# Kernel optimization log

Measured on AMD Instinct MI355X. Metric: run time of the kernel, lower is better.

The kernel has to match this reference:

```python
import jax, jax.numpy as jnp
import numpy as np

L, B, S, D, H, DH, V = 6, 2048, 64, 256, 8, 64, 100
INNER = H * DH          # 512
FF = 4 * D              # 1024 (GeGLU hidden after chunk)
SCALE = 8.0             # sqrt(DH)


def setup_inputs() -> dict:
    key = jax.random.key(0)
    ks = jax.random.split(key, 8)
    s = 0.02
    return {
        "x": jax.random.randint(ks[0], (B, S), 0, V),
        "E": jax.random.normal(ks[1], (S, V, D), dtype=jnp.float32) * s,
        "ln1_g": jnp.ones((L, D), jnp.float32),
        "ln1_b": jnp.zeros((L, D), jnp.float32),
        "Wqkv": jax.random.normal(ks[2], (L, D, 3 * INNER), dtype=jnp.float32) * s,
        "Wout": jax.random.normal(ks[3], (L, INNER, D), dtype=jnp.float32) * s,
        "bout": jnp.zeros((L, D), jnp.float32),
        "ln2_g": jnp.ones((L, D), jnp.float32),
        "ln2_b": jnp.zeros((L, D), jnp.float32),
        "W1": jax.random.normal(ks[4], (L, D, 2 * FF), dtype=jnp.float32) * s,
        "b1": jnp.zeros((L, 2 * FF), jnp.float32),
        "W2": jax.random.normal(ks[5], (L, FF, D), dtype=jnp.float32) * s,
        "b2": jnp.zeros((L, D), jnp.float32),
    }


def _ln(x, g, b):
    m = x.mean(-1, keepdims=True)
    v = ((x - m) ** 2).mean(-1, keepdims=True)
    return (x - m) * jax.lax.rsqrt(v + 1e-5) * g + b


def _split_heads(t):
    # [B,S,H*DH] -> [B,H,S,DH]
    return t.reshape(B, S, H, DH).transpose(0, 2, 1, 3)


def reference(x, E, ln1_g, ln1_b, Wqkv, Wout, bout, ln2_g, ln2_b, W1, b1, W2, b2):
    # per-column embedding lookup: E[col, x[b,col]] -> [B,S,D]
    h = E[jnp.arange(S)[None, :], x]
    for l in range(L):
        # PreNorm -> MHA
        n = _ln(h, ln1_g[l], ln1_b[l])
        qkv = n @ Wqkv[l]
        q, k, v = jnp.split(qkv, 3, axis=-1)
        q, k, v = _split_heads(q), _split_heads(k), _split_heads(v)
        score = jax.nn.softmax(
            jnp.einsum("bhqd,bhkd->bhqk", q, k) / SCALE, axis=-1
        )
        o = jnp.einsum("bhqk,bhkd->bhqd", score, v)
        o = o.transpose(0, 2, 1, 3).reshape(B, S, INNER)
        h = h + o @ Wout[l] + bout[l]
        # PreNorm -> GeGLU FFN
        n2 = _ln(h, ln2_g[l], ln2_b[l])
        u = n2 @ W1[l] + b1[l]
        a, g = jnp.split(u, 2, axis=-1)
        h = (a * jax.nn.gelu(g, approximate=False)) @ W2[l] + b2[l] + h
    return h
```

## Files before the change

### kernel.cpp

```cpp
#include <hip/hip_runtime.h>
#include <stdint.h>
#include <math.h>


#define LAYERS 6
#define BATCH  2048
#define SEQ    64
#define DMODEL 256
#define NHEAD  8
#define INNERD 512
#define FFDIM  1024
#define VOCAB  100
#define MTOK   (BATCH*SEQ)
#define MCAP   65536

typedef unsigned short u16;
typedef __attribute__((ext_vector_type(4))) float f32x4;
typedef __attribute__((ext_vector_type(4))) short s16x4;
typedef __attribute__((ext_vector_type(8))) short s16x8;

__device__ inline u16 f2bf(float f){
  union { float f; unsigned int u; } x; x.f = f;
  unsigned int u = x.u;
  return (u16)((u + 0x7fffu + ((u >> 16) & 1u)) >> 16);
}

__device__ inline void gload16(const void* g, void* l){
  __builtin_amdgcn_global_load_lds(
      (const __attribute__((address_space(1))) unsigned int*)g,
      (__attribute__((address_space(3))) unsigned int*)l, 16, 0, 0);
}

__device__ inline f32x4 mfma16(s16x8 a, s16x8 b, f32x4 c){
  return __builtin_amdgcn_mfma_f32_16x16x32_bf16(a, b, c, 0, 0, 0);
}

__device__ inline s16x8 ldfrag(const u16* lds, int row, int kk, int g){
  int chunk = ((kk<<2)|g) ^ (row&7);
  return *(const s16x8*)(lds + row*64 + chunk*8);
}

__device__ inline s16x8 frag2(const u16* p){
  s16x4 lo = *(const s16x4*)(p);
  s16x4 hi = *(const s16x4*)(p + 16);
  return __builtin_shufflevector(lo, hi, 0,1,2,3,4,5,6,7);
}

__device__ inline int pcol32(int col_base32, int hi, int g, int o){
  return col_base32 | (g<<3) | (hi<<2) | o;
}

__global__ __launch_bounds__(256) void wtrans_kernel(
    const float* __restrict__ in, u16* __restrict__ out, int K, int N, int total)
{
  int idx = blockIdx.x*256 + threadIdx.x;
  if (idx >= total) return;
  int l = idx / (N*K);
  int r = idx - l*(N*K);
  int n = r / K;
  int k = r - n*K;
  int p = (k & ~31) | (((k>>2)&3)<<3) | (((k>>4)&1)<<2) | (k&3);
  out[(size_t)l*N*K + (size_t)n*K + p] = f2bf(in[(size_t)l*K*N + (size_t)k*N + n]);
}

__global__ __launch_bounds__(256) void embed_ln_kernel(
    const int* __restrict__ x, const float* __restrict__ E,
    const float* __restrict__ gam, const float* __restrict__ bet,
    float* __restrict__ h, u16* __restrict__ nout)
{
  int t = threadIdx.x;
  int m = blockIdx.x*4 + (t>>6);
  int lane = t & 63;
  int s = m & 63;
  int tok = x[m];
  const float4 v = *(const float4*)(E + ((size_t)s*VOCAB + tok)*DMODEL + lane*4);
  *(float4*)(h + (size_t)m*DMODEL + lane*4) = v;
  float su = v.x+v.y+v.z+v.w;
  float q  = v.x*v.x+v.y*v.y+v.z*v.z+v.w*v.w;
  #pragma unroll
  for (int mask=1; mask<64; mask<<=1){
    su += __shfl_xor(su, mask);
    q  += __shfl_xor(q,  mask);
  }
  float mean = su*(1.f/256.f);
  float var  = q*(1.f/256.f) - mean*mean;
  float rs   = rsqrtf(var + 1e-5f);
  const float4 gv = *(const float4*)(gam + lane*4);
  const float4 bv = *(const float4*)(bet + lane*4);
  ushort4 ov;
  ov.x = f2bf((v.x-mean)*rs*gv.x + bv.x);
  ov.y = f2bf((v.y-mean)*rs*gv.y + bv.y);
  ov.z = f2bf((v.z-mean)*rs*gv.z + bv.z);
  ov.w = f2bf((v.w-mean)*rs*gv.w + bv.w);
  int p4 = (lane>>3)*32 + (lane&3)*8 + ((lane>>2)&1)*4;
  *(ushort4*)(nout + (size_t)m*DMODEL + p4) = ov;
}

__global__ __launch_bounds__(256, 2) void qkv_attn_kernel(
    const u16* __restrict__ A, const u16* __restrict__ Bt,
    u16* __restrict__ o, int K)
{
  __shared__ __align__(16) u16 smem[38912];
  u16* As = smem;
  u16* Bs = smem + 8192;
  u16* qs = smem;
  u16* ks = smem + 9216;
  u16* vt = smem + 20480;
  u16* ps = smem + 29696;

  const int t = threadIdx.x;
  const int w = t >> 6, lane = t & 63, g = lane >> 4, c = lane & 15;
  const int cpx = gridDim.x >> 3;
  const int wg = (blockIdx.x & 7)*cpx + (blockIdx.x >> 3);
  const int hh = wg & 7;
  const int m0 = (wg >> 3) * 128;

  f32x4 acc[2][12];
  #pragma unroll
  for (int i=0;i<2;++i)
    #pragma unroll
    for (int j=0;j<12;++j){ f32x4 z = {0.f,0.f,0.f,0.f}; acc[i][j] = z; }

  const int nkt = K >> 6;
  for (int kt = 0; kt < nkt; ++kt){
    #pragma unroll
    for (int i=0;i<4;++i){
      int cid = (i*4 + w)*64 + lane;
      int row = cid >> 3, seg = cid & 7;
      gload16(A + (size_t)(m0+row)*K + (size_t)kt*64 + ((seg ^ (row&7))<<3),
              As + cid*8);
    }
    #pragma unroll
    for (int i=0;i<6;++i){
      int cid = (i*4 + w)*64 + lane;
      int brow = cid >> 3, seg = cid & 7;
      int ng = (brow>>6)*512 + hh*64 + (brow & 63);
      gload16(Bt + (size_t)ng*K + (size_t)kt*64 + ((seg ^ (brow&7))<<3),
              Bs + cid*8);
    }
    asm volatile("s_waitcnt vmcnt(0)" ::: "memory");
    __syncthreads();
    #pragma unroll
    for (int kk=0; kk<2; ++kk){
      s16x8 af[2];
      #pragma unroll
      for (int i=0;i<2;++i) af[i] = ldfrag(As, w*32 + i*16 + c, kk, g);
      #pragma unroll
      for (int j=0;j<12;++j){
        s16x8 bf = ldfrag(Bs, j*16 + c, kk, g);
        acc[0][j] = mfma16(af[0], bf, acc[0][j]);
        acc[1][j] = mfma16(af[1], bf, acc[1][j]);
      }
    }
    __syncthreads();
  }

  #pragma unroll
  for (int i=0;i<2;++i){
    #pragma unroll
    for (int j=0;j<12;++j){
      int col = j*16 + c;
      #pragma unroll
      for (int r=0;r<4;++r){
        int tl = w*32 + i*16 + g*4 + r;
        u16 val = f2bf(acc[i][j][r]);
        if (j < 4)       qs[tl*72 + col] = val;
        else if (j < 8)  ks[tl*72 + (col - 64)] = val;
        else             vt[((tl & 64) + col - 128)*72 + (tl & 63)] = val;
      }
    }
  }
  __syncthreads();

  const int seq = w >> 1;
  const u16* qb = qs + (w*32)*72;
  const u16* kb = ks + (seq*64)*72;
  const u16* vb = vt + (seq*64)*72;
  u16* pw = ps + (w*32)*72;

  f32x4 sc[2][4];
  #pragma unroll
  for (int i=0;i<2;++i)
    #pragma unroll
    for (int j=0;j<4;++j){ f32x4 z = {0.f,0.f,0.f,0.f}; sc[i][j] = z; }
  #pragma unroll
  for (int kk=0;kk<2;++kk){
    int k0 = kk*32 + 4*g;
    s16x8 a0 = frag2(qb + (c)*72      + k0);
    s16x8 a1 = frag2(qb + (16 + c)*72 + k0);
    #pragma unroll
    for (int j=0;j<4;++j){
      s16x8 bb = frag2(kb + (j*16 + c)*72 + k0);
      sc[0][j] = mfma16(a0, bb, sc[0][j]);
      sc[1][j] = mfma16(a1, bb, sc[1][j]);
    }
  }

  #pragma unroll
  for (int i=0;i<2;++i){
    #pragma unroll
    for (int r=0;r<4;++r){
      float mx = fmaxf(fmaxf(sc[i][0][r],sc[i][1][r]), fmaxf(sc[i][2][r],sc[i][3][r]));
      #pragma unroll
      for (int mask=1; mask<16; mask<<=1) mx = fmaxf(mx, __shfl_xor(mx, mask));
      float p0 = expf((sc[i][0][r]-mx)*0.125f);
      float p1 = expf((sc[i][1][r]-mx)*0.125f);
      float p2 = expf((sc[i][2][r]-mx)*0.125f);
      float p3 = expf((sc[i][3][r]-mx)*0.125f);
      float sm = p0+p1+p2+p3;
      #pragma unroll
      for (int mask=1; mask<16; mask<<=1) sm += __shfl_xor(sm, mask);
      float inv = 1.f/sm;
      int row = i*16 + g*4 + r;
      pw[row*72 +  0 + c] = f2bf(p0*inv);
      pw[row*72 + 16 + c] = f2bf(p1*inv);
      pw[row*72 + 32 + c] = f2bf(p2*inv);
      pw[row*72 + 48 + c] = f2bf(p3*inv);
    }
  }
  __syncthreads();

  f32x4 oa[2][4];
  #pragma unroll
  for (int i=0;i<2;++i)
    #pragma unroll
    for (int j=0;j<4;++j){ f32x4 z = {0.f,0.f,0.f,0.f}; oa[i][j] = z; }
  #pragma unroll
  for (int kk=0;kk<2;++kk){
    int k0 = kk*32 + 4*g;
    s16x8 a0 = frag2(pw + (c)*72      + k0);
    s16x8 a1 = frag2(pw + (16 + c)*72 + k0);
    #pragma unroll
    for (int j=0;j<4;++j){
      s16x8 bb = frag2(vb + (j*16 + c)*72 + k0);
      oa[0][j] = mfma16(a0, bb, oa[0][j]);
      oa[1][j] = mfma16(a1, bb, oa[1][j]);
    }
  }

  #pragma unroll
  for (int i=0;i<2;++i){
    #pragma unroll
    for (int j=0;j<4;++j){
      int col = hh*64 + j*16 + c;
      int pc = pcol32(col & ~31, j&1, c>>2, c&3);
      #pragma unroll
      for (int r=0;r<4;++r){
        int m = m0 + w*32 + i*16 + g*4 + r;
        o[(size_t)m*INNERD + pc] = f2bf(oa[i][j][r]);
      }
    }
  }
}

__global__ __launch_bounds__(256, 2) void gemm_gated_kernel(
    const u16* __restrict__ A, const u16* __restrict__ Bt,
    u16* __restrict__ act, const float* __restrict__ b1, int K)
{
  __shared__ __align__(16) u16 As[128*64];
  __shared__ __align__(16) u16 Ba[128*64];
  __shared__ __align__(16) u16 Bg[128*64];
  const int t = threadIdx.x;
  const int w = t >> 6, lane = t & 63, g = lane >> 4, c = lane & 15;
  const int cpx = gridDim.x >> 3;
  const int wg = (blockIdx.x & 7)*cpx + (blockIdx.x >> 3);
  const int n0 = (wg & 7) * 128, m0 = (wg >> 3) * 128;
  const int wm = (w >> 1) * 64, wn = (w & 1) * 64;

  f32x4 acca[4][4], accg[4][4];
  #pragma unroll
  for (int i=0;i<4;++i)
    #pragma unroll
    for (int j=0;j<4;++j){ f32x4 z = {0.f,0.f,0.f,0.f}; acca[i][j] = z; accg[i][j] = z; }

  const int nkt = K >> 6;
  for (int kt = 0; kt < nkt; ++kt){
    #pragma unroll
    for (int i=0;i<4;++i){
      int cid = (i*4 + w)*64 + lane;
      int row = cid >> 3, qs = cid & 7;
      int col16 = ((qs ^ (row&7))<<3);
      gload16(A  + (size_t)(m0+row)*K      + (size_t)kt*64 + col16, As + (i*4+w)*512);
      gload16(Bt + (size_t)(n0+row)*K      + (size_t)kt*64 + col16, Ba + (i*4+w)*512);
      gload16(Bt + (size_t)(1024+n0+row)*K + (size_t)kt*64 + col16, Bg + (i*4+w)*512);
    }
    asm volatile("s_waitcnt vmcnt(0)" ::: "memory");
    __syncthreads();
    #pragma unroll
    for (int kk=0; kk<2; ++kk){
      s16x8 af[4];
      #pragma unroll
      for (int i=0;i<4;++i) af[i] = ldfrag(As, wm + i*16 + c, kk, g);
      #pragma unroll
      for (int j=0;j<4;++j){
        int row = wn + j*16 + c;
        s16x8 bfa = ldfrag(Ba, row, kk, g);
        s16x8 bfg = ldfrag(Bg, row, kk, g);
        #pragma unroll
        for (int i=0;i<4;++i){
          acca[i][j] = mfma16(af[i], bfa, acca[i][j]);
          accg[i][j] = mfma16(af[i], bfg, accg[i][j]);
        }
      }
    }
    __syncthreads();
  }

  #pragma unroll
  for (int i=0;i<4;++i)
    #pragma unroll
    for (int j=0;j<4;++j){
      int col = n0 + wn + j*16 + c;
      int pc = pcol32(col & ~31, j&1, c>>2, c&3);
      float ba = b1[col], bg = b1[1024 + col];
      #pragma unroll
      for (int r=0;r<4;++r){
        int m = m0 + wm + i*16 + g*4 + r;
        float ua = acca[i][j][r] + ba;
        float ug = accg[i][j][r] + bg;
        float gel = 0.5f*ug*(1.0f + erff(ug*0.70710678118654752f));
        act[(size_t)m*FFDIM + pc] = f2bf(ua*gel);
      }
    }
}

template<int DO_LN>
__global__ __launch_bounds__(256, 2) void gemm_res_ln_kernel(
    const u16* __restrict__ A, const u16* __restrict__ Bt,
    float* __restrict__ h, const float* __restrict__ bias,
    const float* __restrict__ gam, const float* __restrict__ bet,
    u16* __restrict__ nout, int K)
{
  __shared__ __align__(16) u16 As[128*64];
  __shared__ __align__(16) u16 Bs[256*64];
  __shared__ float ps[128][4];
  const int t = threadIdx.x;
  const int w = t >> 6, lane = t & 63, g = lane >> 4, c = lane & 15;
  const int wr = w >> 1, wc = w & 1;
  const int m0 = blockIdx.x * 128;

  f32x4 acc[4][8];
  #pragma unroll
  for (int i=0;i<4;++i)
    #pragma unroll
    for (int j=0;j<8;++j){ f32x4 z = {0.f,0.f,0.f,0.f}; acc[i][j] = z; }

  const int nkt = K >> 6;
  for (int kt = 0; kt < nkt; ++kt){
    #pragma unroll
    for (int i=0;i<4;++i){
      int cid = (i*4 + w)*64 + lane;
      int row = cid >> 3, qs = cid & 7;
      gload16(A + (size_t)(m0+row)*K + (size_t)kt*64 + ((qs ^ (row&7))<<3),
              As + (i*4+w)*512);
    }
    #pragma unroll
    for (int i=0;i<8;++i){
      int cid = (i*4 + w)*64 + lane;
      int row = cid >> 3, qs = cid & 7;
      gload16(Bt + (size_t)row*K + (size_t)kt*64 + ((qs ^ (row&7))<<3),
              Bs + (i*4+w)*512);
    }
    asm volatile("s_waitcnt vmcnt(0)" ::: "memory");
    __syncthreads();
    #pragma unroll
    for (int kk=0; kk<2; ++kk){
      s16x8 af[4];
      #pragma unroll
      for (int i=0;i<4;++i) af[i] = ldfrag(As, wr*64 + i*16 + c, kk, g);
      #pragma unroll
      for (int j=0;j<8;++j){
        s16x8 bf = ldfrag(Bs, wc*128 + j*16 + c, kk, g);
        #pragma unroll
        for (int i=0;i<4;++i) acc[i][j] = mfma16(af[i], bf, acc[i][j]);
      }
    }
    __syncthreads();
  }

  #pragma unroll
  for (int i=0;i<4;++i){
    #pragma unroll
    for (int r=0;r<4;++r){
      int rl = wr*64 + i*16 + g*4 + r;
      size_t mrow = (size_t)(m0 + rl)*DMODEL;
      float s = 0.f, q2 = 0.f;
      #pragma unroll
      for (int j=0;j<8;++j){
        int col = wc*128 + j*16 + c;
        float v = acc[i][j][r] + bias[col] + h[mrow + col];
        h[mrow + col] = v;
        acc[i][j][r] = v;
        s += v; q2 += v*v;
      }
      if (DO_LN){
        #pragma unroll
        for (int mask=1; mask<16; mask<<=1){
          s  += __shfl_xor(s,  mask);
          q2 += __shfl_xor(q2, mask);
        }
        if (c == 0){ ps[rl][wc*2] = s; ps[rl][wc*2+1] = q2; }
      }
    }
  }
  if (DO_LN){
    __syncthreads();
    #pragma unroll
    for (int i=0;i<4;++i){
      #pragma unroll
      for (int r=0;r<4;++r){
        int rl = wr*64 + i*16 + g*4 + r;
        size_t mrow = (size_t)(m0 + rl)*DMODEL;
        float st = ps[rl][0] + ps[rl][2];
        float qt = ps[rl][1] + ps[rl][3];
        float mean = st*(1.f/256.f);
        float var  = qt*(1.f/256.f) - mean*mean;
        float rs   = rsqrtf(var + 1e-5f);
        #pragma unroll
        for (int j=0;j<8;++j){
          int col = wc*128 + j*16 + c;
          float v = acc[i][j][r];
          int pc = pcol32(col & ~31, j&1, c>>2, c&3);
          nout[mrow + pc] = f2bf((v-mean)*rs*gam[col] + bet[col]);
        }
      }
    }
  }
}

extern "C" void kernel_launch(void* const* d_in, const int* in_sizes, int n_in,
                              void* d_out, int out_size, void* d_ws, size_t ws_size,
                              hipStream_t stream)
{
  const int*   x    = (const int*)  d_in[0];
  const float* E    = (const float*)d_in[1];
  const float* ln1g = (const float*)d_in[2];
  const float* ln1b = (const float*)d_in[3];
  const float* Wqkv = (const float*)d_in[4];
  const float* Wout = (const float*)d_in[5];
  const float* bout = (const float*)d_in[6];
  const float* ln2g = (const float*)d_in[7];
  const float* ln2b = (const float*)d_in[8];
  const float* W1   = (const float*)d_in[9];
  const float* b1   = (const float*)d_in[10];
  const float* W2   = (const float*)d_in[11];
  const float* b2   = (const float*)d_in[12];
  float* h = (float*)d_out;

  const size_t WQKV = (size_t)LAYERS*1536*256;
  const size_t WOUT = (size_t)LAYERS*256*512;
  const size_t W1T  = (size_t)LAYERS*2048*256;
  const size_t W2T  = (size_t)LAYERS*256*1024;
  u16* wqkv_t = (u16*)d_ws;
  u16* wout_t = wqkv_t + WQKV;
  u16* w1_t   = wout_t + WOUT;
  u16* w2_t   = w1_t   + W1T;
  u16* abase  = w2_t   + W2T;
  const size_t wbytes = (WQKV + WOUT + W1T + W2T) * 2;
  if (ws_size < wbytes + (size_t)1024*3584) return;
  size_t rem = ws_size - wbytes;

  int Mc = MCAP;
  while (Mc > 1024 && (size_t)Mc*3584 > rem) Mc >>= 1;
  const int nc = MTOK / Mc;

  u16* n_bf   = abase;
  u16* o_bf   = n_bf + (size_t)Mc*256;
  u16* act_bf = o_bf + (size_t)Mc*512;

  int tot;
  tot = LAYERS*1536*256; wtrans_kernel<<<(tot+255)/256,256,0,stream>>>(Wqkv, wqkv_t, 256,  1536, tot);
  tot = LAYERS*256*512;  wtrans_kernel<<<(tot+255)/256,256,0,stream>>>(Wout, wout_t, 512,  256,  tot);
  tot = LAYERS*2048*256; wtrans_kernel<<<(tot+255)/256,256,0,stream>>>(W1,   w1_t,   256,  2048, tot);
  tot = LAYERS*256*1024; wtrans_kernel<<<(tot+255)/256,256,0,stream>>>(W2,   w2_t,   1024, 256,  tot);

  for (int cidx=0; cidx<nc; ++cidx){
    float* hc = h + (size_t)cidx*Mc*256;
    const int* xc = x + (size_t)cidx*Mc;
    embed_ln_kernel<<<Mc/4,256,0,stream>>>(xc, E, ln1g, ln1b, hc, n_bf);
    for (int l=0; l<LAYERS; ++l){
      qkv_attn_kernel<<<8*(Mc/128),256,0,stream>>>(
          n_bf, wqkv_t + (size_t)l*1536*256, o_bf, 256);
      gemm_res_ln_kernel<1><<<Mc/128,256,0,stream>>>(
          o_bf, wout_t + (size_t)l*256*512, hc, bout + l*256,
          ln2g + l*256, ln2b + l*256, n_bf, 512);
      gemm_gated_kernel<<<8*(Mc/128),256,0,stream>>>(
          n_bf, w1_t + (size_t)l*2048*256, act_bf, b1 + l*2048, 256);
      if (l < LAYERS-1){
        gemm_res_ln_kernel<1><<<Mc/128,256,0,stream>>>(
            act_bf, w2_t + (size_t)l*256*1024, hc, b2 + l*256,
            ln1g + (l+1)*256, ln1b + (l+1)*256, n_bf, 1024);
      } else {
        gemm_res_ln_kernel<0><<<Mc/128,256,0,stream>>>(
            act_bf, w2_t + (size_t)l*256*1024, hc, b2 + l*256,
            nullptr, nullptr, nullptr, 1024);
      }
    }
  }
}
```

Measured before the change: 4.310 ms.

## Keep softmax probabilities in registers, shrink LDS and tiles for higher occupancy

The attention kernel now computes the transposed score (K·Qᵀ), so each lane holds the probabilities for a query column. They are packed straight into bf16 MFMA A-fragments, which removes the LDS staging buffer for P and one barrier. Q, K and V are stored with the swizzled 64-wide LDS layout so ldfrag can be reused, which cuts LDS use enough to allow 3 blocks per CU. The residual+LN GEMM moves from 128-row to 64-row tiles with 3 blocks per CU and twice the grid, and the token chunk cap is halved, trading more launches and more weight re-reads for occupancy and cache locality.

```diff
diff --git a/kernel.cpp b/kernel.cpp
--- a/kernel.cpp
+++ b/kernel.cpp
@@ -12,7 +12,7 @@
 #define FFDIM  1024
 #define VOCAB  100
 #define MTOK   (BATCH*SEQ)
-#define MCAP   65536
+#define MCAP   32768
 
 typedef unsigned short u16;
 typedef __attribute__((ext_vector_type(4))) float f32x4;
@@ -38,12 +38,6 @@
 __device__ inline s16x8 ldfrag(const u16* lds, int row, int kk, int g){
   int chunk = ((kk<<2)|g) ^ (row&7);
   return *(const s16x8*)(lds + row*64 + chunk*8);
-}
-
-__device__ inline s16x8 frag2(const u16* p){
-  s16x4 lo = *(const s16x4*)(p);
-  s16x4 hi = *(const s16x4*)(p + 16);
-  return __builtin_shufflevector(lo, hi, 0,1,2,3,4,5,6,7);
 }
 
 __device__ inline int pcol32(int col_base32, int hi, int g, int o){
@@ -96,17 +90,16 @@
   *(ushort4*)(nout + (size_t)m*DMODEL + p4) = ov;
 }
 
-__global__ __launch_bounds__(256, 2) void qkv_attn_kernel(
+__global__ __launch_bounds__(256, 3) void qkv_attn_kernel(
     const u16* __restrict__ A, const u16* __restrict__ Bt,
     u16* __restrict__ o, int K)
 {
-  __shared__ __align__(16) u16 smem[38912];
+  __shared__ __align__(16) u16 smem[24576];
   u16* As = smem;
   u16* Bs = smem + 8192;
   u16* qs = smem;
-  u16* ks = smem + 9216;
-  u16* vt = smem + 20480;
-  u16* ps = smem + 29696;
+  u16* ks = smem + 8192;
+  u16* vt = smem + 16384;
 
   const int t = threadIdx.x;
   const int w = t >> 6, lane = t & 63, g = lane >> 4, c = lane & 15;
@@ -159,95 +152,102 @@
   for (int i=0;i<2;++i){
     #pragma unroll
     for (int j=0;j<12;++j){
-      int col = j*16 + c;
       #pragma unroll
       for (int r=0;r<4;++r){
         int tl = w*32 + i*16 + g*4 + r;
         u16 val = f2bf(acc[i][j][r]);
-        if (j < 4)       qs[tl*72 + col] = val;
-        else if (j < 8)  ks[tl*72 + (col - 64)] = val;
-        else             vt[((tl & 64) + col - 128)*72 + (tl & 63)] = val;
+        if (j < 8){
+          int chunk = ((j&3)>>1)*4 + (c>>2);
+          int pos   = (j&1)*4 + (c&3);
+          u16* base = (j < 4) ? qs : ks;
+          base[tl*64 + ((chunk ^ (tl&7))<<3) + pos] = val;
+        } else {
+          int d = (j-8)*16 + c;
+          int row = (tl & 64) + d;
+          int kcol = tl & 63;
+          int chunk = ((kcol>>5)<<2) | ((kcol>>2)&3);
+          int pos   = ((kcol>>4)&1)*4 + (kcol&3);
+          vt[row*64 + ((chunk ^ (row&7))<<3) + pos] = val;
+        }
       }
     }
   }
   __syncthreads();
 
   const int seq = w >> 1;
-  const u16* qb = qs + (w*32)*72;
-  const u16* kb = ks + (seq*64)*72;
-  const u16* vb = vt + (seq*64)*72;
-  u16* pw = ps + (w*32)*72;
-
-  f32x4 sc[2][4];
-  #pragma unroll
-  for (int i=0;i<2;++i)
-    #pragma unroll
-    for (int j=0;j<4;++j){ f32x4 z = {0.f,0.f,0.f,0.f}; sc[i][j] = z; }
+  const int qrow = w*32;
+
+  f32x4 sc[4][2];
+  #pragma unroll
+  for (int jk=0;jk<4;++jk){ f32x4 z = {0.f,0.f,0.f,0.f}; sc[jk][0]=z; sc[jk][1]=z; }
   #pragma unroll
   for (int kk=0;kk<2;++kk){
-    int k0 = kk*32 + 4*g;
-    s16x8 a0 = frag2(qb + (c)*72      + k0);
-    s16x8 a1 = frag2(qb + (16 + c)*72 + k0);
-    #pragma unroll
-    for (int j=0;j<4;++j){
-      s16x8 bb = frag2(kb + (j*16 + c)*72 + k0);
-      sc[0][j] = mfma16(a0, bb, sc[0][j]);
-      sc[1][j] = mfma16(a1, bb, sc[1][j]);
-    }
-  }
-
-  #pragma unroll
-  for (int i=0;i<2;++i){
-    #pragma unroll
-    for (int r=0;r<4;++r){
-      float mx = fmaxf(fmaxf(sc[i][0][r],sc[i][1][r]), fmaxf(sc[i][2][r],sc[i][3][r]));
-      #pragma unroll
-      for (int mask=1; mask<16; mask<<=1) mx = fmaxf(mx, __shfl_xor(mx, mask));
-      float p0 = expf((sc[i][0][r]-mx)*0.125f);
-      float p1 = expf((sc[i][1][r]-mx)*0.125f);
-      float p2 = expf((sc[i][2][r]-mx)*0.125f);
-      float p3 = expf((sc[i][3][r]-mx)*0.125f);
-      float sm = p0+p1+p2+p3;
-      #pragma unroll
-      for (int mask=1; mask<16; mask<<=1) sm += __shfl_xor(sm, mask);
-      float inv = 1.f/sm;
-      int row = i*16 + g*4 + r;
-      pw[row*72 +  0 + c] = f2bf(p0*inv);
-      pw[row*72 + 16 + c] = f2bf(p1*inv);
-      pw[row*72 + 32 + c] = f2bf(p2*inv);
-      pw[row*72 + 48 + c] = f2bf(p3*inv);
-    }
-  }
-  __syncthreads();
+    s16x8 qf0 = ldfrag(qs, qrow + c,      kk, g);
+    s16x8 qf1 = ldfrag(qs, qrow + 16 + c, kk, g);
+    #pragma unroll
+    for (int jk=0;jk<4;++jk){
+      s16x8 kf = ldfrag(ks, seq*64 + jk*16 + c, kk, g);
+      sc[jk][0] = mfma16(kf, qf0, sc[jk][0]);
+      sc[jk][1] = mfma16(kf, qf1, sc[jk][1]);
+    }
+  }
+
+  s16x8 af[2][2];
+  #pragma unroll
+  for (int iq=0;iq<2;++iq){
+    float mx = sc[0][iq][0];
+    #pragma unroll
+    for (int jk=0;jk<4;++jk)
+      #pragma unroll
+      for (int r=0;r<4;++r) mx = fmaxf(mx, sc[jk][iq][r]);
+    mx = fmaxf(mx, __shfl_xor(mx, 16));
+    mx = fmaxf(mx, __shfl_xor(mx, 32));
+    float p[4][4];
+    float sm = 0.f;
+    #pragma unroll
+    for (int jk=0;jk<4;++jk)
+      #pragma unroll
+      for (int r=0;r<4;++r){
+        float e = expf((sc[jk][iq][r]-mx)*0.125f);
+        p[jk][r] = e; sm += e;
+      }
+    sm += __shfl_xor(sm, 16);
+    sm += __shfl_xor(sm, 32);
+    float inv = 1.f/sm;
+    #pragma unroll
+    for (int kk=0;kk<2;++kk){
+      union { s16x8 v; u16 e[8]; } u;
+      #pragma unroll
+      for (int oo=0;oo<4;++oo){
+        u.e[oo]   = f2bf(p[2*kk  ][oo]*inv);
+        u.e[4+oo] = f2bf(p[2*kk+1][oo]*inv);
+      }
+      af[iq][kk] = u.v;
+    }
+  }
 
   f32x4 oa[2][4];
   #pragma unroll
-  for (int i=0;i<2;++i)
-    #pragma unroll
-    for (int j=0;j<4;++j){ f32x4 z = {0.f,0.f,0.f,0.f}; oa[i][j] = z; }
-  #pragma unroll
-  for (int kk=0;kk<2;++kk){
-    int k0 = kk*32 + 4*g;
-    s16x8 a0 = frag2(pw + (c)*72      + k0);
-    s16x8 a1 = frag2(pw + (16 + c)*72 + k0);
-    #pragma unroll
-    for (int j=0;j<4;++j){
-      s16x8 bb = frag2(vb + (j*16 + c)*72 + k0);
-      oa[0][j] = mfma16(a0, bb, oa[0][j]);
-      oa[1][j] = mfma16(a1, bb, oa[1][j]);
-    }
-  }
-
-  #pragma unroll
-  for (int i=0;i<2;++i){
-    #pragma unroll
-    for (int j=0;j<4;++j){
-      int col = hh*64 + j*16 + c;
-      int pc = pcol32(col & ~31, j&1, c>>2, c&3);
+  for (int jd=0;jd<4;++jd){ f32x4 z = {0.f,0.f,0.f,0.f}; oa[0][jd]=z; oa[1][jd]=z; }
+  #pragma unroll
+  for (int kk=0;kk<2;++kk)
+    #pragma unroll
+    for (int jd=0;jd<4;++jd){
+      s16x8 vf = ldfrag(vt, seq*64 + jd*16 + c, kk, g);
+      oa[0][jd] = mfma16(af[0][kk], vf, oa[0][jd]);
+      oa[1][jd] = mfma16(af[1][kk], vf, oa[1][jd]);
+    }
+
+  #pragma unroll
+  for (int iq=0;iq<2;++iq){
+    #pragma unroll
+    for (int jd=0;jd<4;++jd){
+      int col = hh*64 + jd*16 + c;
+      int pc = pcol32(col & ~31, jd&1, c>>2, c&3);
       #pragma unroll
       for (int r=0;r<4;++r){
-        int m = m0 + w*32 + i*16 + g*4 + r;
-        o[(size_t)m*INNERD + pc] = f2bf(oa[i][j][r]);
+        int m = m0 + w*32 + iq*16 + g*4 + r;
+        o[(size_t)m*INNERD + pc] = f2bf(oa[iq][jd][r]);
       }
     }
   }
@@ -325,34 +325,34 @@
 }
 
 template<int DO_LN>
-__global__ __launch_bounds__(256, 2) void gemm_res_ln_kernel(
+__global__ __launch_bounds__(256, 3) void gemm_res_ln_kernel(
     const u16* __restrict__ A, const u16* __restrict__ Bt,
     float* __restrict__ h, const float* __restrict__ bias,
     const float* __restrict__ gam, const float* __restrict__ bet,
     u16* __restrict__ nout, int K)
 {
-  __shared__ __align__(16) u16 As[128*64];
+  __shared__ __align__(16) u16 As[64*64];
   __shared__ __align__(16) u16 Bs[256*64];
-  __shared__ float ps[128][4];
+  __shared__ float ps[64][4];
   const int t = threadIdx.x;
   const int w = t >> 6, lane = t & 63, g = lane >> 4, c = lane & 15;
   const int wr = w >> 1, wc = w & 1;
-  const int m0 = blockIdx.x * 128;
-
-  f32x4 acc[4][8];
-  #pragma unroll
-  for (int i=0;i<4;++i)
+  const int m0 = blockIdx.x * 64;
+
+  f32x4 acc[2][8];
+  #pragma unroll
+  for (int i=0;i<2;++i)
     #pragma unroll
     for (int j=0;j<8;++j){ f32x4 z = {0.f,0.f,0.f,0.f}; acc[i][j] = z; }
 
   const int nkt = K >> 6;
   for (int kt = 0; kt < nkt; ++kt){
     #pragma unroll
-    for (int i=0;i<4;++i){
-      int cid = (i*4 + w)*64 + lane;
+    for (int i=0;i<2;++i){
+      int cid = i*256 + t;
       int row = cid >> 3, qs = cid & 7;
       gload16(A + (size_t)(m0+row)*K + (size_t)kt*64 + ((qs ^ (row&7))<<3),
-              As + (i*4+w)*512);
+              As + cid*8);
     }
     #pragma unroll
     for (int i=0;i<8;++i){
@@ -365,24 +365,24 @@
     __syncthreads();
     #pragma unroll
     for (int kk=0; kk<2; ++kk){
-      s16x8 af[4];
-      #pragma unroll
-      for (int i=0;i<4;++i) af[i] = ldfrag(As, wr*64 + i*16 + c, kk, g);
+      s16x8 af[2];
+      #pragma unroll
+      for (int i=0;i<2;++i) af[i] = ldfrag(As, wr*32 + i*16 + c, kk, g);
       #pragma unroll
       for (int j=0;j<8;++j){
         s16x8 bf = ldfrag(Bs, wc*128 + j*16 + c, kk, g);
         #pragma unroll
-        for (int i=0;i<4;++i) acc[i][j] = mfma16(af[i], bf, acc[i][j]);
-      }
-    }
-    __syncthreads();
-  }
-
-  #pragma unroll
-  for (int i=0;i<4;++i){
+        for (int i=0;i<2;++i) acc[i][j] = mfma16(af[i], bf, acc[i][j]);
+      }
+    }
+    __syncthreads();
+  }
+
+  #pragma unroll
+  for (int i=0;i<2;++i){
     #pragma unroll
     for (int r=0;r<4;++r){
-      int rl = wr*64 + i*16 + g*4 + r;
+      int rl = wr*32 + i*16 + g*4 + r;
       size_t mrow = (size_t)(m0 + rl)*DMODEL;
       float s = 0.f, q2 = 0.f;
       #pragma unroll
@@ -406,10 +406,10 @@
   if (DO_LN){
     __syncthreads();
     #pragma unroll
-    for (int i=0;i<4;++i){
+    for (int i=0;i<2;++i){
       #pragma unroll
       for (int r=0;r<4;++r){
-        int rl = wr*64 + i*16 + g*4 + r;
+        int rl = wr*32 + i*16 + g*4 + r;
         size_t mrow = (size_t)(m0 + rl)*DMODEL;
         float st = ps[rl][0] + ps[rl][2];
         float qt = ps[rl][1] + ps[rl][3];
@@ -481,17 +481,17 @@
     for (int l=0; l<LAYERS; ++l){
       qkv_attn_kernel<<<8*(Mc/128),256,0,stream>>>(
           n_bf, wqkv_t + (size_t)l*1536*256, o_bf, 256);
-      gemm_res_ln_kernel<1><<<Mc/128,256,0,stream>>>(
+      gemm_res_ln_kernel<1><<<Mc/64,256,0,stream>>>(
           o_bf, wout_t + (size_t)l*256*512, hc, bout + l*256,
           ln2g + l*256, ln2b + l*256, n_bf, 512);
       gemm_gated_kernel<<<8*(Mc/128),256,0,stream>>>(
           n_bf, w1_t + (size_t)l*2048*256, act_bf, b1 + l*2048, 256);
       if (l < LAYERS-1){
-        gemm_res_ln_kernel<1><<<Mc/128,256,0,stream>>>(
+        gemm_res_ln_kernel<1><<<Mc/64,256,0,stream>>>(
             act_bf, w2_t + (size_t)l*256*1024, hc, b2 + l*256,
             ln1g + (l+1)*256, ln1b + (l+1)*256, n_bf, 1024);
       } else {
-        gemm_res_ln_kernel<0><<<Mc/128,256,0,stream>>>(
+        gemm_res_ln_kernel<0><<<Mc/64,256,0,stream>>>(
             act_bf, w2_t + (size_t)l*256*1024, hc, b2 + l*256,
             nullptr, nullptr, nullptr, 1024);
       }
```

Measured after the change: 3.899 ms. -9.5%, faster.
